# Kernel optimization log

Hardware: AMD Instinct MI355X
Metric: run time of the kernel (lower is better)

Reference implementation:

```python
import jax, jax.numpy as jnp
import numpy as np

B, L, D, H = 4, 1024, 256, 8
TEMP = float(np.sqrt(D))
EPS_SM = 1e-6
EPS_LN = 1e-5


def setup_inputs() -> dict:
    key = jax.random.key(0)
    ks = jax.random.split(key, 8)
    std = float(np.sqrt(2.0 / (D * 2)))
    return {
        "q": jax.random.normal(ks[0], (B, L, D), jnp.float32),
        "mask": jax.random.randint(ks[1], (B, L, L), 0, 2, jnp.int32),
        "k": jax.random.normal(ks[2], (B, L, D), jnp.float32),
        "v": jax.random.normal(ks[3], (B, L, D), jnp.float32),
        "w_qs": jax.random.normal(ks[4], (H * D, D), jnp.float32) * std,
        "w_ks": jax.random.normal(ks[5], (H * D, D), jnp.float32) * std,
        "w_vs": jax.random.normal(ks[6], (H * D, D), jnp.float32) * std,
        "fc_w": jax.random.normal(ks[7], (D, H * D), jnp.float32) * float(np.sqrt(2.0 / (D + H * D))),
        "fc_b": jnp.zeros((D,), jnp.float32),
        "ln_g": jnp.ones((D,), jnp.float32),
        "ln_b": jnp.zeros((D,), jnp.float32),
    }


def masked_softmax(x, m):
    # repo's layers.masked_softmax: clamp, mask-mul, stable exp, mask-mul, normalize
    x = jnp.clip(x, -15.0, 15.0) * m
    e = jnp.exp(x - jnp.max(x, axis=-1, keepdims=True)) * m
    return e / (jnp.sum(e, axis=-1, keepdims=True) + EPS_SM)


def reference(q, mask, k, v, w_qs, w_ks, w_vs, fc_w, fc_b, ln_g, ln_b):
    residual = q
    m = mask.astype(q.dtype)[:, None, :, :]          # [B,1,Lq,Lk]
    # projections to per-head full-dim: [B,L,H,D]
    qh = (q @ w_qs.T).reshape(B, L, H, D)
    kh = (k @ w_ks.T).reshape(B, L, H, D)
    vh = (v @ w_vs.T).reshape(B, L, H, D)
    scores = jnp.einsum("bqhd,bkhd->bhqk", qh, kh) / TEMP   # [B,H,Lq,Lk]
    attn = masked_softmax(scores, m)
    out = jnp.einsum("bhqk,bkhd->bqhd", attn, vh).reshape(B, L, H * D)
    out = out @ fc_w.T + fc_b                         # [B,L,D]
    out = out + residual
    mu = jnp.mean(out, axis=-1, keepdims=True)
    var = jnp.var(out, axis=-1, keepdims=True)
    out = (out - mu) / jnp.sqrt(var + EPS_LN) * ln_g + ln_b
    # match torch attn layout: [H*B, Lq, Lk] (head-major)
    attn_hb = jnp.transpose(attn, (1, 0, 2, 3)).reshape(H * B, L, L)
    return out, attn_hb
```

## Files before the change

kernel.cpp:

```cpp
#include <hip/hip_runtime.h>
#include <cstdint>
#include <math.h>

#define Bsz 4
#define Lsz 1024
#define Dsz 256
#define Hsz 8
#define HD  2048
#define NROWS (Bsz*Lsz)
#define INV_TEMP 0.0625f

typedef __attribute__((ext_vector_type(8))) short bf16x8;
typedef __attribute__((ext_vector_type(4))) float f32x4;

__device__ inline unsigned short f2bf(float f) {
    union { float f; unsigned u; } x; x.f = f;
    unsigned r = x.u + 0x7fffu + ((x.u >> 16) & 1u);
    return (unsigned short)(r >> 16);
}
__device__ inline float bf2f(unsigned short u) {
    union { unsigned u; float f; } x; x.u = (unsigned)u << 16; return x.f;
}

#define GBL(p) ((const __attribute__((address_space(1))) unsigned int*)(p))
#define LDS(p) ((__attribute__((address_space(3))) unsigned int*)(p))

template <int TMv, int TNv, typename OutT, int EPI, int MINW, int DB>
__global__ __launch_bounds__(256, MINW) void gemm_bt(
    const unsigned short* __restrict__ A, const unsigned short* __restrict__ Bm,
    OutT* __restrict__ C,
    int K, int lda, int ldb, int ldc, int inner,
    long long sA1, long long sA2, long long sB1, long long sB2,
    long long sC1, long long sC2, float alpha,
    const unsigned short* __restrict__ maskb, long long sM2,
    const float* __restrict__ invs, long long sI1, long long sI2)
{
    constexpr int WMv = TMv / 2, WNv = TNv / 2;
    constexpr int IT = TMv / 32, JT = TNv / 32;
    constexpr int APASS = TMv / 32, NPASS = (TMv + TNv) / 32;
    constexpr int TILE = (TMv + TNv) * 64;

    const int z  = blockIdx.z;
    const int i1 = z / inner;
    const int i2 = z % inner;
    A  += (size_t)i1 * sA1 + (size_t)i2 * sA2;
    Bm += (size_t)i1 * sB1 + (size_t)i2 * sB2;
    C  += (size_t)i1 * sC1 + (size_t)i2 * sC2;
    if (EPI == 1) maskb += (size_t)i2 * sM2;
    if (EPI == 2) invs  += (size_t)i1 * sI1 + (size_t)i2 * sI2;

    __shared__ unsigned short S[(DB ? 2 : 1) * TILE];

    const int t    = threadIdx.x;
    const int lane = t & 63;
    const int w    = t >> 6;
    const int wm   = w & 1;
    const int wn   = w >> 1;
    const int m0   = blockIdx.x * TMv;
    const int n0   = blockIdx.y * TNv;

    const int rA = t >> 3;
    const int ch = ((t & 7) ^ (rA & 7)) * 8;
    const unsigned short* gA = A  + (size_t)(m0 + rA) * lda + ch;
    const unsigned short* gB = Bm + (size_t)(n0 + rA) * ldb + ch;

    const int fr = lane & 15;
    const int q  = lane >> 4;

    f32x4 acc[IT][JT];
#pragma unroll
    for (int i = 0; i < IT; ++i)
#pragma unroll
        for (int j = 0; j < JT; ++j) acc[i][j] = (f32x4){0.f, 0.f, 0.f, 0.f};

    auto stage = [&](unsigned short* Sb, int k0) {
#pragma unroll
        for (int p = 0; p < NPASS; ++p) {
            const unsigned short* src = (p < APASS)
                ? (gA + (size_t)p * 32 * lda + k0)
                : (gB + (size_t)(p - APASS) * 32 * ldb + k0);
            __builtin_amdgcn_global_load_lds(GBL(src), LDS(Sb + p * 2048 + t * 8), 16, 0, 0);
        }
    };
    auto kstep = [&](const unsigned short* As) {
        const unsigned short* Bs = As + TMv * 64;
#pragma unroll
        for (int ks = 0; ks < 2; ++ks) {
            const int slot = ((ks * 4 + q) ^ (fr & 7)) * 8;
            bf16x8 a[IT], b[JT];
#pragma unroll
            for (int i = 0; i < IT; ++i)
                a[i] = *(const bf16x8*)(As + (wm * WMv + i * 16 + fr) * 64 + slot);
#pragma unroll
            for (int j = 0; j < JT; ++j)
                b[j] = *(const bf16x8*)(Bs + (wn * WNv + j * 16 + fr) * 64 + slot);
#pragma unroll
            for (int i = 0; i < IT; ++i)
#pragma unroll
                for (int j = 0; j < JT; ++j)
                    acc[i][j] = __builtin_amdgcn_mfma_f32_16x16x32_bf16(a[i], b[j], acc[i][j], 0, 0, 0);
        }
    };

    if constexpr (DB) {
        const int nk = K >> 6;
        stage(S, 0);
        __syncthreads();
        int cur = 0;
        for (int kt = 0; kt < nk; ++kt) {
            if (kt + 1 < nk) stage(S + (cur ^ 1) * TILE, (kt + 1) << 6);
            kstep(S + cur * TILE);
            __syncthreads();
            cur ^= 1;
        }
    } else {
        for (int k0 = 0; k0 < K; k0 += 64) {
            stage(S, k0);
            __syncthreads();
            kstep(S);
            __syncthreads();
        }
    }

#pragma unroll
    for (int i = 0; i < IT; ++i) {
#pragma unroll
        for (int r = 0; r < 4; ++r) {
            const int row = m0 + wm * WMv + i * 16 + q * 4 + r;
#pragma unroll
            for (int j = 0; j < JT; ++j) {
                const int col = n0 + wn * WNv + j * 16 + fr;
                float vv = acc[i][j][r] * alpha;
                if (EPI == 0) {
                    if constexpr (sizeof(OutT) == 4)
                        C[(size_t)row * ldc + col] = (OutT)vv;
                    else
                        ((unsigned short*)C)[(size_t)row * ldc + col] = f2bf(vv);
                } else if (EPI == 1) {
                    const float m = bf2f(maskb[(size_t)row * Lsz + col]);
                    vv = fminf(fmaxf(vv, -15.f), 15.f) * m;
                    vv = __expf(vv) * m;
                    ((unsigned short*)C)[(size_t)row * ldc + col] = f2bf(vv);
                } else {
                    vv *= invs[row];
                    ((unsigned short*)C)[(size_t)row * ldc + col] = f2bf(vv);
                }
            }
        }
    }
}

__global__ __launch_bounds__(256) void cast_all(
    const float* __restrict__ q, const float* __restrict__ k, const float* __restrict__ v,
    const float* __restrict__ wq, const float* __restrict__ wk, const float* __restrict__ wv,
    const float* __restrict__ fw, const int* __restrict__ mask,
    unsigned short* __restrict__ qb, unsigned short* __restrict__ kb, unsigned short* __restrict__ vb,
    unsigned short* __restrict__ wqb, unsigned short* __restrict__ wkb, unsigned short* __restrict__ wvb,
    unsigned short* __restrict__ fwb, unsigned short* __restrict__ mb)
{
    const int gid = blockIdx.x * 256 + threadIdx.x;
    const int NQ = 262144;
    const int NW = 131072;
    const int NF = 3 * NQ + 4 * NW;
    if (gid >= NF) {
        const int off = gid - NF;
        const int4 mi = ((const int4*)mask)[off];
        ushort4 o;
        o.x = mi.x ? 0x3F80 : 0;
        o.y = mi.y ? 0x3F80 : 0;
        o.z = mi.z ? 0x3F80 : 0;
        o.w = mi.w ? 0x3F80 : 0;
        ((ushort4*)mb)[off] = o;
        return;
    }
    const float* src; unsigned short* dst; int off;
    if      (gid < NQ)            { src = q;  dst = qb;  off = gid; }
    else if (gid < 2 * NQ)        { src = k;  dst = kb;  off = gid - NQ; }
    else if (gid < 3 * NQ)        { src = v;  dst = vb;  off = gid - 2 * NQ; }
    else if (gid < 3 * NQ + NW)   { src = wq; dst = wqb; off = gid - 3 * NQ; }
    else if (gid < 3 * NQ + 2*NW) { src = wk; dst = wkb; off = gid - 3 * NQ - NW; }
    else if (gid < 3 * NQ + 3*NW) { src = wv; dst = wvb; off = gid - 3 * NQ - 2 * NW; }
    else                          { src = fw; dst = fwb; off = gid - 3 * NQ - 3 * NW; }
    float4 f = ((const float4*)src)[off];
    ushort4 o;
    o.x = f2bf(f.x); o.y = f2bf(f.y); o.z = f2bf(f.z); o.w = f2bf(f.w);
    ((ushort4*)dst)[off] = o;
}

__global__ __launch_bounds__(256) void norm_kernel(const unsigned short* __restrict__ e,
                                                   float* __restrict__ attn,
                                                   float* __restrict__ invsum)
{
    const int r    = blockIdx.x * 4 + (threadIdx.x >> 6);
    const int lane = threadIdx.x & 63;
    const unsigned short* rowp = e + (size_t)r * Lsz + lane * 16;

    union { uint4 v[2]; unsigned short u[16]; } buf;
    buf.v[0] = *(const uint4*)rowp;
    buf.v[1] = *(const uint4*)(rowp + 8);

    float f[16];
    float s = 0.f;
#pragma unroll
    for (int i = 0; i < 16; ++i) { f[i] = bf2f(buf.u[i]); s += f[i]; }
#pragma unroll
    for (int o = 1; o <= 32; o <<= 1) s += __shfl_xor(s, o, 64);
    const float inv = 1.0f / (s + 1e-6f);

    float* op = attn + (size_t)r * Lsz + lane * 16;
#pragma unroll
    for (int c = 0; c < 4; ++c) {
        float4 o4;
        o4.x = f[c * 4 + 0] * inv; o4.y = f[c * 4 + 1] * inv;
        o4.z = f[c * 4 + 2] * inv; o4.w = f[c * 4 + 3] * inv;
        *(float4*)(op + c * 4) = o4;
    }
    if (lane == 0) invsum[r] = inv;
}

__global__ __launch_bounds__(256) void ln_kernel(const float* __restrict__ gout,
                                                 const float* __restrict__ qin,
                                                 const float* __restrict__ fc_b,
                                                 const float* __restrict__ ln_g,
                                                 const float* __restrict__ ln_b,
                                                 float* __restrict__ out)
{
    const int row = blockIdx.x;
    const int t = threadIdx.x;
    const size_t idx = (size_t)row * Dsz + t;
    const size_t P = (size_t)NROWS * Dsz;
    const float val = gout[idx] + gout[idx + P] + gout[idx + 2 * P] + gout[idx + 3 * P]
                    + fc_b[t] + qin[idx];

    __shared__ float red[4];
    float s = val;
#pragma unroll
    for (int o = 32; o > 0; o >>= 1) s += __shfl_down(s, o, 64);
    const int lane = t & 63, w = t >> 6;
    if (lane == 0) red[w] = s;
    __syncthreads();
    const float mu = (red[0] + red[1] + red[2] + red[3]) * (1.0f / Dsz);
    __syncthreads();

    float d = val - mu;
    float s2 = d * d;
#pragma unroll
    for (int o = 32; o > 0; o >>= 1) s2 += __shfl_down(s2, o, 64);
    if (lane == 0) red[w] = s2;
    __syncthreads();
    const float var = (red[0] + red[1] + red[2] + red[3]) * (1.0f / Dsz);

    out[idx] = d * rsqrtf(var + 1e-5f) * ln_g[t] + ln_b[t];
}

extern "C" void kernel_launch(void* const* d_in, const int* in_sizes, int n_in,
                              void* d_out, int out_size, void* d_ws, size_t ws_size,
                              hipStream_t stream)
{
    const float* q    = (const float*)d_in[0];
    const int*   mask = (const int*)d_in[1];
    const float* k    = (const float*)d_in[2];
    const float* v    = (const float*)d_in[3];
    const float* w_qs = (const float*)d_in[4];
    const float* w_ks = (const float*)d_in[5];
    const float* w_vs = (const float*)d_in[6];
    const float* fc_w = (const float*)d_in[7];
    const float* fc_b = (const float*)d_in[8];
    const float* ln_g = (const float*)d_in[9];
    const float* ln_b = (const float*)d_in[10];

    float* out  = (float*)d_out;
    float* attn = (float*)d_out + (size_t)NROWS * Dsz;

    unsigned short* wsu = (unsigned short*)d_ws;
    unsigned short* qh     = wsu;
    unsigned short* kh     = qh + (size_t)NROWS * HD;
    unsigned short* q_bf   = kh + (size_t)NROWS * HD;
    unsigned short* k_bf   = q_bf + (size_t)NROWS * Dsz;
    unsigned short* v_bf   = k_bf + (size_t)NROWS * Dsz;
    unsigned short* wq_bf  = v_bf + (size_t)NROWS * Dsz;
    unsigned short* wk_bf  = wq_bf + (size_t)HD * Dsz;
    unsigned short* wv_bf  = wk_bf + (size_t)HD * Dsz;
    unsigned short* vt     = wv_bf + (size_t)HD * Dsz;
    unsigned short* attn_e = vt + (size_t)Bsz * HD * Lsz;
    unsigned short* attnv  = attn_e + (size_t)32 * Lsz * Lsz;
    unsigned short* fcw_bf = attnv + (size_t)NROWS * HD;
    float*          invsum = (float*)(fcw_bf + (size_t)Dsz * HD);
    float*          fcout  = invsum + 32768;
    unsigned short* maskb  = (unsigned short*)(fcout + (size_t)4 * NROWS * Dsz);

    dim3 blk(256);

    cast_all<<<dim3(9216), blk, 0, stream>>>(q, k, v, w_qs, w_ks, w_vs, fc_w, mask,
                                             q_bf, k_bf, v_bf, wq_bf, wk_bf, wv_bf, fcw_bf, maskb);

    {
        dim3 grid(NROWS / 128, HD / 128, 2);
        gemm_bt<128, 128, unsigned short, 0, 3, 0><<<grid, blk, 0, stream>>>(q_bf, wq_bf, qh,
            Dsz, Dsz, Dsz, HD, 2,
            0, (long long)NROWS * Dsz, 0, (long long)HD * Dsz, 0, (long long)NROWS * HD,
            1.0f, nullptr, 0, nullptr, 0, 0);
    }

    {
        dim3 grid(HD / 128, Lsz / 128, Bsz);
        gemm_bt<128, 128, unsigned short, 0, 2, 1><<<grid, blk, 0, stream>>>(wv_bf, v_bf, vt,
            Dsz, Dsz, Dsz, Lsz, 1,
            0, 0, (long long)Lsz * Dsz, 0, (long long)HD * Lsz, 0,
            1.0f, nullptr, 0, nullptr, 0, 0);
    }

    {
        dim3 grid(Lsz / 128, Lsz / 128, Hsz * Bsz);
        gemm_bt<128, 128, unsigned short, 1, 3, 0><<<grid, blk, 0, stream>>>(qh, kh, attn_e,
            Dsz, HD, HD, Lsz, Bsz,
            Dsz, (long long)Lsz * HD, Dsz, (long long)Lsz * HD,
            (long long)Bsz * Lsz * Lsz, (long long)Lsz * Lsz,
            INV_TEMP, maskb, (long long)Lsz * Lsz, nullptr, 0, 0);
    }

    norm_kernel<<<dim3(32 * Lsz / 4), blk, 0, stream>>>(attn_e, attn, invsum);

    {
        dim3 grid(Lsz / 128, Dsz / 128, Hsz * Bsz);
        gemm_bt<128, 128, unsigned short, 2, 2, 1><<<grid, blk, 0, stream>>>(attn_e, vt, attnv,
            Lsz, Lsz, Lsz, HD, Bsz,
            (long long)Bsz * Lsz * Lsz, (long long)Lsz * Lsz,
            (long long)Dsz * Lsz, (long long)HD * Lsz,
            Dsz, (long long)Lsz * HD,
            1.0f, nullptr, 0, invsum, (long long)Bsz * Lsz, (long long)Lsz);
    }

    {
        dim3 grid(NROWS / 64, Dsz / 128, 4);
        gemm_bt<64, 128, float, 0, 3, 1><<<grid, blk, 0, stream>>>(attnv, fcw_bf, fcout,
            512, HD, HD, Dsz, 4,
            0, 512, 0, 512, 0, (long long)NROWS * Dsz,
            1.0f, nullptr, 0, nullptr, 0, 0);
    }

    ln_kernel<<<dim3(NROWS), blk, 0, stream>>>(fcout, q, fc_b, ln_g, ln_b, out);
}
```

Baseline: 336.8 us.

## Fuse softmax row-sum into score GEMM and normalization into PV GEMM

Drops the standalone normalization kernel. The score GEMM epilogue now reduces each row's partial exp sum across lanes and accumulates it with atomics into a row-sum buffer, which the cast kernel zeroes beforehand. The PV GEMM computes reciprocal sums in LDS, scales its output, and also writes the normalized fp32 attention matrix by re-reading the bf16 exp tile, each y-block covering half the columns. This removes one full read of the unnormalized tile and a kernel launch, at the cost of atomics and extra global traffic inside the PV GEMM epilogue.

```diff
diff --git a/kernel.cpp b/kernel.cpp
--- a/kernel.cpp
+++ b/kernel.cpp
@@ -33,7 +33,8 @@
     long long sA1, long long sA2, long long sB1, long long sB2,
     long long sC1, long long sC2, float alpha,
     const unsigned short* __restrict__ maskb, long long sM2,
-    const float* __restrict__ invs, long long sI1, long long sI2)
+    const float* __restrict__ invs, long long sI1, long long sI2,
+    float* __restrict__ aux)
 {
     constexpr int WMv = TMv / 2, WNv = TNv / 2;
     constexpr int IT = TMv / 32, JT = TNv / 32;
@@ -46,10 +47,11 @@
     A  += (size_t)i1 * sA1 + (size_t)i2 * sA2;
     Bm += (size_t)i1 * sB1 + (size_t)i2 * sB2;
     C  += (size_t)i1 * sC1 + (size_t)i2 * sC2;
-    if (EPI == 1) maskb += (size_t)i2 * sM2;
-    if (EPI == 2) invs  += (size_t)i1 * sI1 + (size_t)i2 * sI2;
+    if (EPI == 1) { maskb += (size_t)i2 * sM2; aux += (size_t)z * Lsz; }
+    if (EPI == 2) { invs  += (size_t)i1 * sI1 + (size_t)i2 * sI2; aux += (size_t)z * Lsz * Lsz; }
 
     __shared__ unsigned short S[(DB ? 2 : 1) * TILE];
+    __shared__ float inv_lds[EPI == 2 ? TMv : 1];
 
     const int t    = threadIdx.x;
     const int lane = t & 63;
@@ -122,11 +124,17 @@
         }
     }
 
+    if constexpr (EPI == 2) {
+        if (t < TMv) inv_lds[t] = 1.0f / (invs[m0 + t] + 1e-6f);
+        __syncthreads();
+    }
+
 #pragma unroll
     for (int i = 0; i < IT; ++i) {
 #pragma unroll
         for (int r = 0; r < 4; ++r) {
             const int row = m0 + wm * WMv + i * 16 + q * 4 + r;
+            float rsum = 0.f;
 #pragma unroll
             for (int j = 0; j < JT; ++j) {
                 const int col = n0 + wn * WNv + j * 16 + fr;
@@ -140,12 +148,38 @@
                     const float m = bf2f(maskb[(size_t)row * Lsz + col]);
                     vv = fminf(fmaxf(vv, -15.f), 15.f) * m;
                     vv = __expf(vv) * m;
-                    ((unsigned short*)C)[(size_t)row * ldc + col] = f2bf(vv);
+                    const unsigned short us = f2bf(vv);
+                    ((unsigned short*)C)[(size_t)row * ldc + col] = us;
+                    rsum += bf2f(us);
                 } else {
-                    vv *= invs[row];
+                    vv *= inv_lds[row - m0];
                     ((unsigned short*)C)[(size_t)row * ldc + col] = f2bf(vv);
                 }
             }
+            if constexpr (EPI == 1) {
+#pragma unroll
+                for (int o = 1; o <= 8; o <<= 1) rsum += __shfl_xor(rsum, o, 64);
+                if (fr == 0) atomicAdd(&aux[row], rsum);
+            }
+        }
+    }
+
+    if constexpr (EPI == 2) {
+        const int c0 = blockIdx.y * (Lsz / 2);
+#pragma unroll 4
+        for (int rr = 0; rr < TMv / 4; ++rr) {
+            const int rl = rr * 4 + w;
+            const float iv = inv_lds[rl];
+            const unsigned short* ep = A + (size_t)(m0 + rl) * lda + c0 + lane * 8;
+            const uint4 u = *(const uint4*)ep;
+            float4 lo, hi;
+            lo.x = bf2f((unsigned short)(u.x & 0xffff)) * iv; lo.y = bf2f((unsigned short)(u.x >> 16)) * iv;
+            lo.z = bf2f((unsigned short)(u.y & 0xffff)) * iv; lo.w = bf2f((unsigned short)(u.y >> 16)) * iv;
+            hi.x = bf2f((unsigned short)(u.z & 0xffff)) * iv; hi.y = bf2f((unsigned short)(u.z >> 16)) * iv;
+            hi.z = bf2f((unsigned short)(u.w & 0xffff)) * iv; hi.w = bf2f((unsigned short)(u.w >> 16)) * iv;
+            float* op = aux + (size_t)(m0 + rl) * Lsz + c0 + lane * 8;
+            *(float4*)op = lo;
+            *(float4*)(op + 4) = hi;
         }
     }
 }
@@ -156,14 +190,21 @@
     const float* __restrict__ fw, const int* __restrict__ mask,
     unsigned short* __restrict__ qb, unsigned short* __restrict__ kb, unsigned short* __restrict__ vb,
     unsigned short* __restrict__ wqb, unsigned short* __restrict__ wkb, unsigned short* __restrict__ wvb,
-    unsigned short* __restrict__ fwb, unsigned short* __restrict__ mb)
+    unsigned short* __restrict__ fwb, unsigned short* __restrict__ mb,
+    float* __restrict__ rs)
 {
     const int gid = blockIdx.x * 256 + threadIdx.x;
     const int NQ = 262144;
     const int NW = 131072;
     const int NF = 3 * NQ + 4 * NW;
+    const int NM = 1048576;
     if (gid >= NF) {
         const int off = gid - NF;
+        if (off >= NM) {
+            const int ri = off - NM;
+            if (ri < 8192) ((float4*)rs)[ri] = (float4){0.f, 0.f, 0.f, 0.f};
+            return;
+        }
         const int4 mi = ((const int4*)mask)[off];
         ushort4 o;
         o.x = mi.x ? 0x3F80 : 0;
@@ -185,37 +226,6 @@
     ushort4 o;
     o.x = f2bf(f.x); o.y = f2bf(f.y); o.z = f2bf(f.z); o.w = f2bf(f.w);
     ((ushort4*)dst)[off] = o;
-}
-
-__global__ __launch_bounds__(256) void norm_kernel(const unsigned short* __restrict__ e,
-                                                   float* __restrict__ attn,
-                                                   float* __restrict__ invsum)
-{
-    const int r    = blockIdx.x * 4 + (threadIdx.x >> 6);
-    const int lane = threadIdx.x & 63;
-    const unsigned short* rowp = e + (size_t)r * Lsz + lane * 16;
-
-    union { uint4 v[2]; unsigned short u[16]; } buf;
-    buf.v[0] = *(const uint4*)rowp;
-    buf.v[1] = *(const uint4*)(rowp + 8);
-
-    float f[16];
-    float s = 0.f;
-#pragma unroll
-    for (int i = 0; i < 16; ++i) { f[i] = bf2f(buf.u[i]); s += f[i]; }
-#pragma unroll
-    for (int o = 1; o <= 32; o <<= 1) s += __shfl_xor(s, o, 64);
-    const float inv = 1.0f / (s + 1e-6f);
-
-    float* op = attn + (size_t)r * Lsz + lane * 16;
-#pragma unroll
-    for (int c = 0; c < 4; ++c) {
-        float4 o4;
-        o4.x = f[c * 4 + 0] * inv; o4.y = f[c * 4 + 1] * inv;
-        o4.z = f[c * 4 + 2] * inv; o4.w = f[c * 4 + 3] * inv;
-        *(float4*)(op + c * 4) = o4;
-    }
-    if (lane == 0) invsum[r] = inv;
 }
 
 __global__ __launch_bounds__(256) void ln_kernel(const float* __restrict__ gout,
@@ -285,21 +295,22 @@
     unsigned short* attn_e = vt + (size_t)Bsz * HD * Lsz;
     unsigned short* attnv  = attn_e + (size_t)32 * Lsz * Lsz;
     unsigned short* fcw_bf = attnv + (size_t)NROWS * HD;
-    float*          invsum = (float*)(fcw_bf + (size_t)Dsz * HD);
-    float*          fcout  = invsum + 32768;
+    float*          rowsum = (float*)(fcw_bf + (size_t)Dsz * HD);
+    float*          fcout  = rowsum + 32768;
     unsigned short* maskb  = (unsigned short*)(fcout + (size_t)4 * NROWS * Dsz);
 
     dim3 blk(256);
 
-    cast_all<<<dim3(9216), blk, 0, stream>>>(q, k, v, w_qs, w_ks, w_vs, fc_w, mask,
-                                             q_bf, k_bf, v_bf, wq_bf, wk_bf, wv_bf, fcw_bf, maskb);
+    cast_all<<<dim3(9248), blk, 0, stream>>>(q, k, v, w_qs, w_ks, w_vs, fc_w, mask,
+                                             q_bf, k_bf, v_bf, wq_bf, wk_bf, wv_bf, fcw_bf, maskb,
+                                             rowsum);
 
     {
         dim3 grid(NROWS / 128, HD / 128, 2);
         gemm_bt<128, 128, unsigned short, 0, 3, 0><<<grid, blk, 0, stream>>>(q_bf, wq_bf, qh,
             Dsz, Dsz, Dsz, HD, 2,
             0, (long long)NROWS * Dsz, 0, (long long)HD * Dsz, 0, (long long)NROWS * HD,
-            1.0f, nullptr, 0, nullptr, 0, 0);
+            1.0f, nullptr, 0, nullptr, 0, 0, nullptr);
     }
 
     {
@@ -307,7 +318,7 @@
         gemm_bt<128, 128, unsigned short, 0, 2, 1><<<grid, blk, 0, stream>>>(wv_bf, v_bf, vt,
             Dsz, Dsz, Dsz, Lsz, 1,
             0, 0, (long long)Lsz * Dsz, 0, (long long)HD * Lsz, 0,
-            1.0f, nullptr, 0, nullptr, 0, 0);
+            1.0f, nullptr, 0, nullptr, 0, 0, nullptr);
     }
 
     {
@@ -316,10 +327,8 @@
             Dsz, HD, HD, Lsz, Bsz,
             Dsz, (long long)Lsz * HD, Dsz, (long long)Lsz * HD,
             (long long)Bsz * Lsz * Lsz, (long long)Lsz * Lsz,
-            INV_TEMP, maskb, (long long)Lsz * Lsz, nullptr, 0, 0);
-    }
-
-    norm_kernel<<<dim3(32 * Lsz / 4), blk, 0, stream>>>(attn_e, attn, invsum);
+            INV_TEMP, maskb, (long long)Lsz * Lsz, nullptr, 0, 0, rowsum);
+    }
 
     {
         dim3 grid(Lsz / 128, Dsz / 128, Hsz * Bsz);
@@ -328,7 +337,7 @@
             (long long)Bsz * Lsz * Lsz, (long long)Lsz * Lsz,
             (long long)Dsz * Lsz, (long long)HD * Lsz,
             Dsz, (long long)Lsz * HD,
-            1.0f, nullptr, 0, invsum, (long long)Bsz * Lsz, (long long)Lsz);
+            1.0f, nullptr, 0, rowsum, (long long)Bsz * Lsz, (long long)Lsz, attn);
     }
 
     {
@@ -336,7 +345,7 @@
         gemm_bt<64, 128, float, 0, 3, 1><<<grid, blk, 0, stream>>>(attnv, fcw_bf, fcout,
             512, HD, HD, Dsz, 4,
             0, 512, 0, 512, 0, (long long)NROWS * Dsz,
-            1.0f, nullptr, 0, nullptr, 0, 0);
+            1.0f, nullptr, 0, nullptr, 0, 0, nullptr);
     }
 
     ln_kernel<<<dim3(NROWS), blk, 0, stream>>>(fcout, q, fc_b, ln_g, ln_b, out);
```

Result: slower. 370.7 us (+10.1%).
